# Kernel tuning notes

Measured on AMD Instinct MI355X. Metric: run time of the kernel, lower is better.

The kernel has to match this reference:

```python
import jax, jax.numpy as jnp
import numpy as np

N = 2_000_000
NUM_PTS = 500_000
NUM_GROUPS = 10_000
NUM_POSITIONS = 8
NUM_CAMS = 8


def _quat_mul(q1, q2):
    """Hamilton product, quaternions stored [x, y, z, w] (pypose convention)."""
    v1, w1 = q1[..., :3], q1[..., 3:4]
    v2, w2 = q2[..., :3], q2[..., 3:4]
    w = w1 * w2 - jnp.sum(v1 * v2, axis=-1, keepdims=True)
    v = w1 * v2 + w2 * v1 + jnp.cross(v1, v2)
    return jnp.concatenate([v, w], axis=-1)


def _quat_rotate(q, p):
    """Rotate points p [...,3] by unit quaternion q [...,4] ([x,y,z,w])."""
    v, w = q[..., :3], q[..., 3:4]
    uv = jnp.cross(v, p)
    uuv = jnp.cross(v, uv)
    return p + 2.0 * (w * uv + uuv)


def _random_se3(key, n, rot_scale=0.1, trans_scale=0.5):
    kq, kt = jax.random.split(key)
    qv = rot_scale * jax.random.normal(kq, (n, 3), dtype=jnp.float32)
    qw = jnp.ones((n, 1), dtype=jnp.float32)
    q = jnp.concatenate([qv, qw], axis=-1)
    q = q / jnp.linalg.norm(q, axis=-1, keepdims=True)
    t = trans_scale * jax.random.normal(kt, (n, 3), dtype=jnp.float32)
    return jnp.concatenate([t, q], axis=-1)  # [n,7] = [tx,ty,tz,qx,qy,qz,qw]


def setup_inputs() -> dict:
    key = jax.random.key(0)
    ks = jax.random.split(key, 10)
    points_2d = 1000.0 * jax.random.uniform(ks[0], (N, 2), dtype=jnp.float32)
    camera_indices = jax.random.randint(ks[1], (N,), 0, NUM_CAMS)
    group_idx = jax.random.randint(ks[2], (N,), 0, NUM_GROUPS)
    member_idx = jax.random.randint(ks[3], (N,), 0, NUM_POSITIONS)
    grouping_indices = jnp.stack([group_idx, member_idx], axis=-1)  # [N,2]
    point_indices = jax.random.randint(ks[4], (N,), 0, NUM_PTS)
    camera_pps = 500.0 + 10.0 * jax.random.normal(ks[5], (NUM_CAMS, 2), dtype=jnp.float32)
    intrs = 1000.0 + 50.0 * jax.random.normal(ks[6], (NUM_CAMS, 2), dtype=jnp.float32)
    # 3D points in front of the rig: z in [4, 10) to keep projection well-conditioned
    xy = 2.0 * jax.random.normal(ks[7], (NUM_PTS, 2), dtype=jnp.float32)
    z = 4.0 + 6.0 * jax.random.uniform(ks[8], (NUM_PTS, 1), dtype=jnp.float32)
    points_3d = jnp.concatenate([xy, z], axis=-1)
    kref, krel = jax.random.split(ks[9])
    ref_poses = _random_se3(kref, NUM_GROUPS)
    rel_poses = _random_se3(krel, NUM_POSITIONS, rot_scale=0.05, trans_scale=0.2)
    return {
        "points_2d": points_2d,
        "camera_indices": camera_indices,
        "grouping_indices": grouping_indices,
        "point_indices": point_indices,
        "camera_pps": camera_pps,
        "intrs": intrs,
        "points_3d": points_3d,
        "ref_poses": ref_poses,
        "rel_poses": rel_poses,
    }


def reference(points_2d, camera_indices, grouping_indices, point_indices,
              camera_pps, intrs, points_3d, ref_poses, rel_poses):
    group_idx = grouping_indices[:, 0]
    member_idx = grouping_indices[:, 1]
    ref = ref_poses[group_idx]    # [N,7]
    rel = rel_poses[member_idx]   # [N,7]
    # SE3 compose: image_pose = rel @ ref  ->  (t_rel + R_rel * t_ref, q_rel * q_ref)
    t = rel[:, :3] + _quat_rotate(rel[:, 3:], ref[:, :3])
    q = _quat_mul(rel[:, 3:], ref[:, 3:])
    # Transform points into camera frame and project (pinhole)
    p_cam = _quat_rotate(q, points_3d[point_indices]) + t  # [N,3]
    uv = intrs[camera_indices] * (p_cam[:, :2] / p_cam[:, 2:3]) + camera_pps[camera_indices]
    return uv - points_2d  # [N,2] reprojection residual
```

## Files before the change

### kernel.cpp

```cpp
#include <hip/hip_runtime.h>


typedef float f4 __attribute__((ext_vector_type(4)));

enum { NGRP = 10000 };

__global__ __launch_bounds__(256) void repack_ref_kernel(
    const float* __restrict__ ref_poses,
    f4* __restrict__ ws)
{
    int g = blockIdx.x * blockDim.x + threadIdx.x;
    if (g >= NGRP) return;
    const float* rp = ref_poses + 7 * g;
    f4 a; a.x = rp[0]; a.y = rp[1]; a.z = rp[2]; a.w = rp[3];
    f4 b; b.x = rp[4]; b.y = rp[5]; b.z = rp[6]; b.w = 0.0f;
    ws[2 * g]     = a;
    ws[2 * g + 1] = b;
}

__global__ __launch_bounds__(256) void reproj_kernel(
    const float2* __restrict__ points_2d,
    const int*    __restrict__ camera_indices,
    const int2*   __restrict__ grouping_indices,
    const int*    __restrict__ point_indices,
    const float*  __restrict__ camera_pps,
    const float*  __restrict__ intrs,
    const float*  __restrict__ points_3d,
    const f4*     __restrict__ refpk,
    const float*  __restrict__ rel_poses,
    float2*       __restrict__ out,
    int n)
{
    __shared__ float s_rel[56];
    __shared__ float s_pps[16];
    __shared__ float s_intr[16];
    int tid = threadIdx.x;
    if (tid < 56) s_rel[tid] = rel_poses[tid];
    if (tid < 16) { s_pps[tid] = camera_pps[tid]; s_intr[tid] = intrs[tid]; }
    __syncthreads();

    int i = blockIdx.x * blockDim.x + tid;
    if (i >= n) return;

    int2  gm  = grouping_indices[i];
    int   pi  = point_indices[i];
    int   cam = camera_indices[i];
    float2 p2d = points_2d[i];

    f4 ca = refpk[2 * gm.x];
    f4 cb = refpk[2 * gm.x + 1];
    float rtx = ca.x, rty = ca.y, rtz = ca.z;
    float rqx = ca.w, rqy = cb.x, rqz = cb.y, rqw = cb.z;

    const float* lp = s_rel + 7 * gm.y;
    float ltx = lp[0], lty = lp[1], ltz = lp[2];
    float lqx = lp[3], lqy = lp[4], lqz = lp[5], lqw = lp[6];

    float uvx = lqy * rtz - lqz * rty;
    float uvy = lqz * rtx - lqx * rtz;
    float uvz = lqx * rty - lqy * rtx;
    float uuvx = lqy * uvz - lqz * uvy;
    float uuvy = lqz * uvx - lqx * uvz;
    float uuvz = lqx * uvy - lqy * uvx;
    float tx = ltx + rtx + 2.0f * (lqw * uvx + uuvx);
    float ty = lty + rty + 2.0f * (lqw * uvy + uuvy);
    float tz = ltz + rtz + 2.0f * (lqw * uvz + uuvz);

    float qw = lqw * rqw - (lqx * rqx + lqy * rqy + lqz * rqz);
    float qx = lqw * rqx + rqw * lqx + (lqy * rqz - lqz * rqy);
    float qy = lqw * rqy + rqw * lqy + (lqz * rqx - lqx * rqz);
    float qz = lqw * rqz + rqw * lqz + (lqx * rqy - lqy * rqx);

    const float* pp = points_3d + 3 * pi;
    float px = pp[0], py = pp[1], pz = pp[2];

    float v2x = qy * pz - qz * py;
    float v2y = qz * px - qx * pz;
    float v2z = qx * py - qy * px;
    float w2x = qy * v2z - qz * v2y;
    float w2y = qz * v2x - qx * v2z;
    float w2z = qx * v2y - qy * v2x;
    float pcx = px + 2.0f * (qw * v2x + w2x) + tx;
    float pcy = py + 2.0f * (qw * v2y + w2y) + ty;
    float pcz = pz + 2.0f * (qw * v2z + w2z) + tz;

    float invz = 1.0f / pcz;
    float ux = s_intr[2 * cam]     * (pcx * invz) + s_pps[2 * cam];
    float uy = s_intr[2 * cam + 1] * (pcy * invz) + s_pps[2 * cam + 1];

    out[i] = make_float2(ux - p2d.x, uy - p2d.y);
}

__global__ __launch_bounds__(256) void reproj_inline_kernel(
    const float2* __restrict__ points_2d,
    const int*    __restrict__ camera_indices,
    const int2*   __restrict__ grouping_indices,
    const int*    __restrict__ point_indices,
    const float*  __restrict__ camera_pps,
    const float*  __restrict__ intrs,
    const float*  __restrict__ points_3d,
    const float*  __restrict__ ref_poses,
    const float*  __restrict__ rel_poses,
    float2*       __restrict__ out,
    int n)
{
    __shared__ float s_rel[56];
    __shared__ float s_pps[16];
    __shared__ float s_intr[16];
    int tid = threadIdx.x;
    if (tid < 56) s_rel[tid] = rel_poses[tid];
    if (tid < 16) { s_pps[tid] = camera_pps[tid]; s_intr[tid] = intrs[tid]; }
    __syncthreads();

    int i = blockIdx.x * blockDim.x + tid;
    if (i >= n) return;

    int2  gm  = grouping_indices[i];
    int   pi  = point_indices[i];
    int   cam = camera_indices[i];
    float2 p2d = points_2d[i];

    const float* rp = ref_poses + 7 * gm.x;
    float rtx = rp[0], rty = rp[1], rtz = rp[2];
    float rqx = rp[3], rqy = rp[4], rqz = rp[5], rqw = rp[6];
    const float* lp = s_rel + 7 * gm.y;
    float ltx = lp[0], lty = lp[1], ltz = lp[2];
    float lqx = lp[3], lqy = lp[4], lqz = lp[5], lqw = lp[6];

    float uvx = lqy * rtz - lqz * rty;
    float uvy = lqz * rtx - lqx * rtz;
    float uvz = lqx * rty - lqy * rtx;
    float uuvx = lqy * uvz - lqz * uvy;
    float uuvy = lqz * uvx - lqx * uvz;
    float uuvz = lqx * uvy - lqy * uvx;
    float tx = ltx + rtx + 2.0f * (lqw * uvx + uuvx);
    float ty = lty + rty + 2.0f * (lqw * uvy + uuvy);
    float tz = ltz + rtz + 2.0f * (lqw * uvz + uuvz);

    float qw = lqw * rqw - (lqx * rqx + lqy * rqy + lqz * rqz);
    float qx = lqw * rqx + rqw * lqx + (lqy * rqz - lqz * rqy);
    float qy = lqw * rqy + rqw * lqy + (lqz * rqx - lqx * rqz);
    float qz = lqw * rqz + rqw * lqz + (lqx * rqy - lqy * rqx);

    const float* pp = points_3d + 3 * pi;
    float px = pp[0], py = pp[1], pz = pp[2];

    float v2x = qy * pz - qz * py;
    float v2y = qz * px - qx * pz;
    float v2z = qx * py - qy * px;
    float w2x = qy * v2z - qz * v2y;
    float w2y = qz * v2x - qx * v2z;
    float w2z = qx * v2y - qy * v2x;
    float pcx = px + 2.0f * (qw * v2x + w2x) + tx;
    float pcy = py + 2.0f * (qw * v2y + w2y) + ty;
    float pcz = pz + 2.0f * (qw * v2z + w2z) + tz;

    float invz = 1.0f / pcz;
    float ux = s_intr[2 * cam]     * (pcx * invz) + s_pps[2 * cam];
    float uy = s_intr[2 * cam + 1] * (pcy * invz) + s_pps[2 * cam + 1];

    out[i] = make_float2(ux - p2d.x, uy - p2d.y);
}

extern "C" void kernel_launch(void* const* d_in, const int* in_sizes, int n_in,
                              void* d_out, int out_size, void* d_ws, size_t ws_size,
                              hipStream_t stream) {
    const float2* points_2d       = (const float2*)d_in[0];
    const int*    camera_indices  = (const int*)d_in[1];
    const int2*   grouping        = (const int2*)d_in[2];
    const int*    point_indices   = (const int*)d_in[3];
    const float*  camera_pps      = (const float*)d_in[4];
    const float*  intrs           = (const float*)d_in[5];
    const float*  points_3d       = (const float*)d_in[6];
    const float*  ref_poses       = (const float*)d_in[7];
    const float*  rel_poses       = (const float*)d_in[8];
    float2*       out             = (float2*)d_out;

    int n = in_sizes[1];
    int blocks = (n + 255) / 256;

    size_t need = (size_t)NGRP * 32;
    if (d_ws && ws_size >= need) {
        f4* ws = (f4*)d_ws;
        repack_ref_kernel<<<(NGRP + 255) / 256, 256, 0, stream>>>(ref_poses, ws);
        reproj_kernel<<<blocks, 256, 0, stream>>>(
            points_2d, camera_indices, grouping, point_indices,
            camera_pps, intrs, points_3d, ws, rel_poses, out, n);
    } else {
        reproj_inline_kernel<<<blocks, 256, 0, stream>>>(
            points_2d, camera_indices, grouping, point_indices,
            camera_pps, intrs, points_3d, ref_poses, rel_poses, out, n);
    }
}
```

Measured before the change: 132.8 us.

## Fuse ref-pose repack and reprojection into one cooperative grid-synced kernel

Replaces the two-kernel sequence (repack of ref poses into aligned float4 workspace, then reprojection) with a single cooperative kernel. The grid is sized to occupancy, does the repack in a grid-stride loop, then a grid-wide sync, then a grid-stride loop over the reprojection. This removes one kernel launch and the gap between kernels, at the cost of a grid barrier, a persistent-style grid-stride loop, and cooperative launch overhead.

Result: slower. 244.7 us (+84.3%).

```diff
diff --git a/kernel.cpp b/kernel.cpp
--- a/kernel.cpp
+++ b/kernel.cpp
@@ -1,9 +1,99 @@
 #include <hip/hip_runtime.h>
-
+#include <hip/hip_cooperative_groups.h>
+
+
+namespace cg = cooperative_groups;
 
 typedef float f4 __attribute__((ext_vector_type(4)));
 
 enum { NGRP = 10000 };
+
+__global__ __launch_bounds__(256) void fused_kernel(
+    const float2* __restrict__ points_2d,
+    const int*    __restrict__ camera_indices,
+    const int2*   __restrict__ grouping_indices,
+    const int*    __restrict__ point_indices,
+    const float*  __restrict__ camera_pps,
+    const float*  __restrict__ intrs,
+    const float*  __restrict__ points_3d,
+    const float*  __restrict__ ref_poses,
+    const float*  __restrict__ rel_poses,
+    f4*           __restrict__ ws,
+    float2*       __restrict__ out,
+    int n)
+{
+    __shared__ float s_rel[56];
+    __shared__ float s_pps[16];
+    __shared__ float s_intr[16];
+    int tid = threadIdx.x;
+    if (tid < 56) s_rel[tid] = rel_poses[tid];
+    if (tid < 16) { s_pps[tid] = camera_pps[tid]; s_intr[tid] = intrs[tid]; }
+    __syncthreads();
+
+    int gsize = gridDim.x * blockDim.x;
+    int gtid  = blockIdx.x * blockDim.x + tid;
+
+    for (int g = gtid; g < NGRP; g += gsize) {
+        const float* rp = ref_poses + 7 * g;
+        f4 a; a.x = rp[0]; a.y = rp[1]; a.z = rp[2]; a.w = rp[3];
+        f4 b; b.x = rp[4]; b.y = rp[5]; b.z = rp[6]; b.w = 0.0f;
+        ws[2 * g]     = a;
+        ws[2 * g + 1] = b;
+    }
+
+    __threadfence();
+    cg::this_grid().sync();
+
+    for (int i = gtid; i < n; i += gsize) {
+        int2  gm  = grouping_indices[i];
+        int   pi  = point_indices[i];
+        int   cam = camera_indices[i];
+        float2 p2d = points_2d[i];
+
+        f4 ca = ws[2 * gm.x];
+        f4 cb = ws[2 * gm.x + 1];
+        float rtx = ca.x, rty = ca.y, rtz = ca.z;
+        float rqx = ca.w, rqy = cb.x, rqz = cb.y, rqw = cb.z;
+
+        const float* lp = s_rel + 7 * gm.y;
+        float ltx = lp[0], lty = lp[1], ltz = lp[2];
+        float lqx = lp[3], lqy = lp[4], lqz = lp[5], lqw = lp[6];
+
+        float uvx = lqy * rtz - lqz * rty;
+        float uvy = lqz * rtx - lqx * rtz;
+        float uvz = lqx * rty - lqy * rtx;
+        float uuvx = lqy * uvz - lqz * uvy;
+        float uuvy = lqz * uvx - lqx * uvz;
+        float uuvz = lqx * uvy - lqy * uvx;
+        float tx = ltx + rtx + 2.0f * (lqw * uvx + uuvx);
+        float ty = lty + rty + 2.0f * (lqw * uvy + uuvy);
+        float tz = ltz + rtz + 2.0f * (lqw * uvz + uuvz);
+
+        float qw = lqw * rqw - (lqx * rqx + lqy * rqy + lqz * rqz);
+        float qx = lqw * rqx + rqw * lqx + (lqy * rqz - lqz * rqy);
+        float qy = lqw * rqy + rqw * lqy + (lqz * rqx - lqx * rqz);
+        float qz = lqw * rqz + rqw * lqz + (lqx * rqy - lqy * rqx);
+
+        const float* pp = points_3d + 3 * pi;
+        float px = pp[0], py = pp[1], pz = pp[2];
+
+        float v2x = qy * pz - qz * py;
+        float v2y = qz * px - qx * pz;
+        float v2z = qx * py - qy * px;
+        float w2x = qy * v2z - qz * v2y;
+        float w2y = qz * v2x - qx * v2z;
+        float w2z = qx * v2y - qy * v2x;
+        float pcx = px + 2.0f * (qw * v2x + w2x) + tx;
+        float pcy = py + 2.0f * (qw * v2y + w2y) + ty;
+        float pcz = pz + 2.0f * (qw * v2z + w2z) + tz;
+
+        float invz = 1.0f / pcz;
+        float ux = s_intr[2 * cam]     * (pcx * invz) + s_pps[2 * cam];
+        float uy = s_intr[2 * cam + 1] * (pcy * invz) + s_pps[2 * cam + 1];
+
+        out[i] = make_float2(ux - p2d.x, uy - p2d.y);
+    }
+}
 
 __global__ __launch_bounds__(256) void repack_ref_kernel(
     const float* __restrict__ ref_poses,
@@ -177,16 +267,45 @@
     float2*       out             = (float2*)d_out;
 
     int n = in_sizes[1];
-    int blocks = (n + 255) / 256;
-
     size_t need = (size_t)NGRP * 32;
+
     if (d_ws && ws_size >= need) {
         f4* ws = (f4*)d_ws;
+
+        static int coopBlocks = -1;
+        if (coopBlocks < 0) {
+            int perCU = 0, nCU = 0;
+            hipError_t e1 = hipOccupancyMaxActiveBlocksPerMultiprocessor(
+                &perCU, (const void*)fused_kernel, 256, 0);
+            hipDeviceProp_t prop;
+            hipError_t e2 = hipGetDeviceProperties(&prop, 0);
+            if (e2 == hipSuccess) nCU = prop.multiProcessorCount;
+            coopBlocks = (e1 == hipSuccess && perCU > 0 && nCU > 0)
+                             ? perCU * nCU : 0;
+        }
+
+        if (coopBlocks > 0) {
+            int blocks = coopBlocks;
+            int maxUseful = (n + 255) / 256;
+            if (blocks > maxUseful) blocks = maxUseful;
+            void* args[] = {
+                (void*)&points_2d, (void*)&camera_indices, (void*)&grouping,
+                (void*)&point_indices, (void*)&camera_pps, (void*)&intrs,
+                (void*)&points_3d, (void*)&ref_poses, (void*)&rel_poses,
+                (void*)&ws, (void*)&out, (void*)&n };
+            hipError_t err = hipLaunchCooperativeKernel(
+                (const void*)fused_kernel, dim3(blocks), dim3(256),
+                args, 0, stream);
+            if (err == hipSuccess) return;
+        }
+
+        int blocks = (n + 255) / 256;
         repack_ref_kernel<<<(NGRP + 255) / 256, 256, 0, stream>>>(ref_poses, ws);
         reproj_kernel<<<blocks, 256, 0, stream>>>(
             points_2d, camera_indices, grouping, point_indices,
             camera_pps, intrs, points_3d, ws, rel_poses, out, n);
     } else {
+        int blocks = (n + 255) / 256;
         reproj_inline_kernel<<<blocks, 256, 0, stream>>>(
             points_2d, camera_indices, grouping, point_indices,
             camera_pps, intrs, points_3d, ref_poses, rel_poses, out, n);
```
